# Kernel optimization log

Measured on AMD Instinct MI355X. Metric: run time of the kernel, lower is better.

## Reference

```python
import jax, jax.numpy as jnp
import numpy as np

F = 16      # frames
NV = 4096   # visual points per frame
NT = 512    # tactile points per frame
M = 4096    # model points
SCALE = 0.1


def setup_inputs() -> dict:
    key = jax.random.key(0)
    ks = jax.random.split(key, 6)
    return {
        "state": jax.random.normal(ks[0], (6,), dtype=jnp.float32) * 0.1,
        "model_points": jax.random.normal(ks[1], (M, 3), dtype=jnp.float32),
        "visual_points": jax.random.normal(ks[2], (F, NV, 3), dtype=jnp.float32),
        "tactile_points": jax.random.normal(ks[3], (F, NT, 3), dtype=jnp.float32),
        "physics_pred_states": jax.random.normal(ks[4], (F, 12), dtype=jnp.float32) * 0.1,
        "delta_time": jax.random.uniform(ks[5], (F,), dtype=jnp.float32, minval=0.01, maxval=0.05),
    }


def _skew(a):
    z = jnp.zeros((), a.dtype)
    return jnp.array([[z, -a[2], a[1]],
                      [a[2], z, -a[0]],
                      [-a[1], a[0], z]])


def _rot_from_omega(omega, dt):
    # Rodrigues: R = I + sin(theta*dt) S + (1 - cos(theta*dt)) S@S, S = skew(omega/|omega|)
    theta = jnp.linalg.norm(omega)
    ax = omega / jnp.clip(theta, 1e-8)
    S = _skew(ax)
    return jnp.eye(3, dtype=omega.dtype) + jnp.sin(theta * dt) * S + (1.0 - jnp.cos(theta * dt)) * (S @ S)


def _chamfer(pred, gt):
    # rows: pred [N,3], cols: gt [M,3]; row-min of squared distances, then mean
    d = (jnp.sum(pred * pred, axis=1)[:, None]
         + jnp.sum(gt * gt, axis=1)[None, :]
         - 2.0 * pred @ gt.T)
    return jnp.mean(jnp.min(d, axis=1))


def reference(state, model_points, visual_points, tactile_points, physics_pred_states, delta_time):
    t0 = state[:3]
    r0 = _rot_from_omega(state[3:], jnp.float32(1.0))  # Euler2Mat modeled as axis-angle

    def pose_step(carry, x):
        t, r = carry
        v, omega, dt = x
        t = t + v * dt
        r = _rot_from_omega(omega, dt) @ r
        return (t, r), (t, r)

    _, (ts, rs) = jax.lax.scan(
        pose_step, (t0, r0),
        (physics_pred_states[1:, 6:9], physics_pred_states[1:, 9:12], delta_time[1:]))
    ts = jnp.concatenate([t0[None], ts], axis=0)  # [F,3]
    rs = jnp.concatenate([r0[None], rs], axis=0)  # [F,3,3]

    def frame_loss(acc, x):
        t, r, vp, tp = x
        vc = ((vp - t) @ r) / SCALE
        tc = ((tp - t) @ r) / SCALE
        acc = acc + _chamfer(vc, model_points) + 0.1 * _chamfer(tc, model_points)
        return acc, None

    E_cd, _ = jax.lax.scan(frame_loss, jnp.zeros((), jnp.float32),
                           (ts, rs, visual_points, tactile_points))
    return E_cd
```

## Files before the change

### kernel.cpp

```cpp
#include <hip/hip_runtime.h>
#include <math.h>

#define F_    16
#define NV_   4096
#define NT_   512
#define M_    4096
#define PPF_  (NV_ + NT_)
#define NPTS_ (F_ * PPF_)
#define SCALE_INV 10.0f

#define TPB    256
#define PPT    4
#define PPB    (TPB * PPT)
#define NPB    (NPTS_ / PPB)
#define CHUNK  256
#define NCHUNK (M_ / CHUNK)

__device__ inline void rot_from_omega(float ox, float oy, float oz, float dt,
                                      float* R) {
    float theta = sqrtf(ox * ox + oy * oy + oz * oz);
    float inv = 1.0f / fmaxf(theta, 1e-8f);
    float ax = ox * inv, ay = oy * inv, az = oz * inv;
    float s = sinf(theta * dt);
    float c = 1.0f - cosf(theta * dt);
    R[0] = 1.0f - c * (ay * ay + az * az);
    R[1] = -s * az + c * ax * ay;
    R[2] =  s * ay + c * ax * az;
    R[3] =  s * az + c * ax * ay;
    R[4] = 1.0f - c * (ax * ax + az * az);
    R[5] = -s * ax + c * ay * az;
    R[6] = -s * ay + c * ax * az;
    R[7] =  s * ax + c * ay * az;
    R[8] = 1.0f - c * (ax * ax + ay * ay);
}

__device__ inline void compute_pose(int f, const float* state, const float* phys,
                                    const float* dts, float* t, float* R) {
    t[0] = state[0]; t[1] = state[1]; t[2] = state[2];
    rot_from_omega(state[3], state[4], state[5], 1.0f, R);
    for (int i = 1; i <= f; ++i) {
        float dt = dts[i];
        t[0] += phys[i * 12 + 6] * dt;
        t[1] += phys[i * 12 + 7] * dt;
        t[2] += phys[i * 12 + 8] * dt;
        float Rs[9];
        rot_from_omega(phys[i * 12 + 9], phys[i * 12 + 10], phys[i * 12 + 11], dt, Rs);
        float Rn[9];
        for (int r = 0; r < 3; ++r)
            for (int c2 = 0; c2 < 3; ++c2)
                Rn[r * 3 + c2] = Rs[r * 3 + 0] * R[0 + c2] +
                                 Rs[r * 3 + 1] * R[3 + c2] +
                                 Rs[r * 3 + 2] * R[6 + c2];
        for (int j = 0; j < 9; ++j) R[j] = Rn[j];
    }
}

__global__ void pose_kernel(const float* __restrict__ state,
                            const float* __restrict__ phys,
                            const float* __restrict__ dts,
                            float* __restrict__ poses) {
    int f = threadIdx.x;
    if (f < F_) {
        float t[3], R[9];
        compute_pose(f, state, phys, dts, t, R);
        float* o = poses + f * 12;
        o[0] = t[0]; o[1] = t[1]; o[2] = t[2];
        for (int j = 0; j < 9; ++j) o[3 + j] = R[j];
    }
}

__global__ __launch_bounds__(TPB) void chamfer_main(
    const float* __restrict__ model, const float* __restrict__ vis,
    const float* __restrict__ tac, const float* __restrict__ poses,
    float* __restrict__ partials) {
    __shared__ float4 sfeat[CHUNK];
    const int pb = blockIdx.x;
    const int ch = blockIdx.y;
    const int mbase = ch * CHUNK;

    for (int i = threadIdx.x; i < CHUNK; i += TPB) {
        float gx = model[(mbase + i) * 3 + 0];
        float gy = model[(mbase + i) * 3 + 1];
        float gz = model[(mbase + i) * 3 + 2];
        sfeat[i] = make_float4(-2.0f * gx, -2.0f * gy, -2.0f * gz,
                               gx * gx + gy * gy + gz * gz);
    }

    float c0[PPT], c1[PPT], c2[PPT], cn[PPT], dm[PPT];
    int pts[PPT];
#pragma unroll
    for (int k = 0; k < PPT; ++k) {
        int pt = pb * PPB + k * TPB + threadIdx.x;
        pts[k] = pt;
        int f = pt / PPF_;
        int loc = pt - f * PPF_;
        const float* p = (loc < NV_) ? (vis + ((size_t)f * NV_ + loc) * 3)
                                     : (tac + ((size_t)f * NT_ + (loc - NV_)) * 3);
        float px = p[0], py = p[1], pz = p[2];
        const float* ps = poses + f * 12;
        float d0 = px - ps[0], d1 = py - ps[1], d2 = pz - ps[2];
        const float* R = ps + 3;
        float x = (d0 * R[0] + d1 * R[3] + d2 * R[6]) * SCALE_INV;
        float y = (d0 * R[1] + d1 * R[4] + d2 * R[7]) * SCALE_INV;
        float z = (d0 * R[2] + d1 * R[5] + d2 * R[8]) * SCALE_INV;
        c0[k] = x; c1[k] = y; c2[k] = z;
        cn[k] = x * x + y * y + z * z;
        dm[k] = 3.4e38f;
    }
    __syncthreads();

#pragma unroll 2
    for (int m = 0; m < CHUNK; m += 2) {
        float4 ga = sfeat[m];
        float4 gb = sfeat[m + 1];
#pragma unroll
        for (int k = 0; k < PPT; ++k) {
            float da = fmaf(ga.x, c0[k], fmaf(ga.y, c1[k], fmaf(ga.z, c2[k], ga.w)));
            float db = fmaf(gb.x, c0[k], fmaf(gb.y, c1[k], fmaf(gb.z, c2[k], gb.w)));
            dm[k] = fminf(dm[k], fminf(da, db));
        }
    }

#pragma unroll
    for (int k = 0; k < PPT; ++k)
        partials[(size_t)ch * NPTS_ + pts[k]] = dm[k] + cn[k];
}

__global__ __launch_bounds__(TPB) void chamfer_reduce(
    const float* __restrict__ partials, float* __restrict__ out) {
    int pt = blockIdx.x * TPB + threadIdx.x;
    float m = partials[pt];
    for (int ch = 1; ch < NCHUNK; ++ch)
        m = fminf(m, partials[(size_t)ch * NPTS_ + pt]);
    int loc = pt % PPF_;
    float w = (loc < NV_) ? (1.0f / NV_) : (0.1f / NT_);
    float v = m * w;
#pragma unroll
    for (int off = 32; off > 0; off >>= 1) v += __shfl_down(v, off);
    __shared__ float sw[TPB / 64];
    if ((threadIdx.x & 63) == 0) sw[threadIdx.x >> 6] = v;
    __syncthreads();
    if (threadIdx.x == 0) {
        float s = 0.0f;
        for (int i = 0; i < TPB / 64; ++i) s += sw[i];
        atomicAdd(out, s);
    }
}

__global__ __launch_bounds__(TPB) void chamfer_fused(
    const float* __restrict__ state, const float* __restrict__ model,
    const float* __restrict__ vis, const float* __restrict__ tac,
    const float* __restrict__ phys, const float* __restrict__ dts,
    float* __restrict__ out) {
    __shared__ float4 sfeat[CHUNK];
    __shared__ float sposes[F_ * 12];
    __shared__ float sw[TPB / 64];

    if (threadIdx.x < F_) {
        float t[3], R[9];
        compute_pose(threadIdx.x, state, phys, dts, t, R);
        float* o = sposes + threadIdx.x * 12;
        o[0] = t[0]; o[1] = t[1]; o[2] = t[2];
        for (int j = 0; j < 9; ++j) o[3 + j] = R[j];
    }
    __syncthreads();

    float c0[PPT], c1[PPT], c2[PPT], cn[PPT], dm[PPT], wt[PPT];
#pragma unroll
    for (int k = 0; k < PPT; ++k) {
        int pt = blockIdx.x * PPB + k * TPB + threadIdx.x;
        int f = pt / PPF_;
        int loc = pt - f * PPF_;
        wt[k] = (loc < NV_) ? (1.0f / NV_) : (0.1f / NT_);
        const float* p = (loc < NV_) ? (vis + ((size_t)f * NV_ + loc) * 3)
                                     : (tac + ((size_t)f * NT_ + (loc - NV_)) * 3);
        float px = p[0], py = p[1], pz = p[2];
        const float* ps = sposes + f * 12;
        float d0 = px - ps[0], d1 = py - ps[1], d2 = pz - ps[2];
        const float* R = ps + 3;
        float x = (d0 * R[0] + d1 * R[3] + d2 * R[6]) * SCALE_INV;
        float y = (d0 * R[1] + d1 * R[4] + d2 * R[7]) * SCALE_INV;
        float z = (d0 * R[2] + d1 * R[5] + d2 * R[8]) * SCALE_INV;
        c0[k] = x; c1[k] = y; c2[k] = z;
        cn[k] = x * x + y * y + z * z;
        dm[k] = 3.4e38f;
    }

    for (int ch = 0; ch < NCHUNK; ++ch) {
        __syncthreads();
        for (int i = threadIdx.x; i < CHUNK; i += TPB) {
            int mi = ch * CHUNK + i;
            float gx = model[mi * 3 + 0], gy = model[mi * 3 + 1], gz = model[mi * 3 + 2];
            sfeat[i] = make_float4(-2.0f * gx, -2.0f * gy, -2.0f * gz,
                                   gx * gx + gy * gy + gz * gz);
        }
        __syncthreads();
#pragma unroll 2
        for (int m = 0; m < CHUNK; m += 2) {
            float4 ga = sfeat[m];
            float4 gb = sfeat[m + 1];
#pragma unroll
            for (int k = 0; k < PPT; ++k) {
                float da = fmaf(ga.x, c0[k], fmaf(ga.y, c1[k], fmaf(ga.z, c2[k], ga.w)));
                float db = fmaf(gb.x, c0[k], fmaf(gb.y, c1[k], fmaf(gb.z, c2[k], gb.w)));
                dm[k] = fminf(dm[k], fminf(da, db));
            }
        }
    }

    float v = 0.0f;
#pragma unroll
    for (int k = 0; k < PPT; ++k) v += (dm[k] + cn[k]) * wt[k];
#pragma unroll
    for (int off = 32; off > 0; off >>= 1) v += __shfl_down(v, off);
    if ((threadIdx.x & 63) == 0) sw[threadIdx.x >> 6] = v;
    __syncthreads();
    if (threadIdx.x == 0) {
        float s = 0.0f;
        for (int i = 0; i < TPB / 64; ++i) s += sw[i];
        atomicAdd(out, s);
    }
}

extern "C" void kernel_launch(void* const* d_in, const int* in_sizes, int n_in,
                              void* d_out, int out_size, void* d_ws, size_t ws_size,
                              hipStream_t stream) {
    const float* state = (const float*)d_in[0];
    const float* model = (const float*)d_in[1];
    const float* vis   = (const float*)d_in[2];
    const float* tac   = (const float*)d_in[3];
    const float* phys  = (const float*)d_in[4];
    const float* dts   = (const float*)d_in[5];
    float* out = (float*)d_out;

    hipMemsetAsync(out, 0, sizeof(float), stream);

    const size_t partial_bytes = (size_t)NCHUNK * NPTS_ * sizeof(float);
    const size_t need = partial_bytes + F_ * 12 * sizeof(float);

    if (ws_size >= need) {
        float* partials = (float*)d_ws;
        float* poses = (float*)((char*)d_ws + partial_bytes);
        pose_kernel<<<1, 64, 0, stream>>>(state, phys, dts, poses);
        dim3 grid(NPB, NCHUNK);
        chamfer_main<<<grid, TPB, 0, stream>>>(model, vis, tac, poses, partials);
        chamfer_reduce<<<NPTS_ / TPB, TPB, 0, stream>>>(partials, out);
    } else {
        chamfer_fused<<<NPB, TPB, 0, stream>>>(state, model, vis, tac, phys, dts, out);
    }
}
```

Before: 107.4 us.

## Fold pose computation into chamfer kernel and retile points per thread and chunks

Removes the separate pose kernel launch: each chamfer_main block now computes all frame poses into shared memory itself. Points per thread double to raise register reuse of each shared model point, and the model chunk halves, so the grid gains twice as many chunk blocks along y. The partials buffer grows accordingly and the reduce kernel reads twice as many chunk partials per point. Redundant per-block pose computation and higher register pressure are the costs.

```diff
diff --git a/kernel.cpp b/kernel.cpp
--- a/kernel.cpp
+++ b/kernel.cpp
@@ -10,10 +10,10 @@
 #define SCALE_INV 10.0f
 
 #define TPB    256
-#define PPT    4
+#define PPT    8
 #define PPB    (TPB * PPT)
 #define NPB    (NPTS_ / PPB)
-#define CHUNK  256
+#define CHUNK  128
 #define NCHUNK (M_ / CHUNK)
 
 __device__ inline void rot_from_omega(float ox, float oy, float oz, float dt,
@@ -55,49 +55,45 @@
     }
 }
 
-__global__ void pose_kernel(const float* __restrict__ state,
-                            const float* __restrict__ phys,
-                            const float* __restrict__ dts,
-                            float* __restrict__ poses) {
-    int f = threadIdx.x;
-    if (f < F_) {
-        float t[3], R[9];
-        compute_pose(f, state, phys, dts, t, R);
-        float* o = poses + f * 12;
-        o[0] = t[0]; o[1] = t[1]; o[2] = t[2];
-        for (int j = 0; j < 9; ++j) o[3 + j] = R[j];
-    }
-}
-
 __global__ __launch_bounds__(TPB) void chamfer_main(
-    const float* __restrict__ model, const float* __restrict__ vis,
-    const float* __restrict__ tac, const float* __restrict__ poses,
+    const float* __restrict__ state, const float* __restrict__ model,
+    const float* __restrict__ vis, const float* __restrict__ tac,
+    const float* __restrict__ phys, const float* __restrict__ dts,
     float* __restrict__ partials) {
     __shared__ float4 sfeat[CHUNK];
+    __shared__ float sposes[F_ * 12];
     const int pb = blockIdx.x;
     const int ch = blockIdx.y;
     const int mbase = ch * CHUNK;
 
-    for (int i = threadIdx.x; i < CHUNK; i += TPB) {
+    if (threadIdx.x < F_) {
+        float t[3], R[9];
+        compute_pose(threadIdx.x, state, phys, dts, t, R);
+        float* o = sposes + threadIdx.x * 12;
+        o[0] = t[0]; o[1] = t[1]; o[2] = t[2];
+        for (int j = 0; j < 9; ++j) o[3 + j] = R[j];
+    }
+
+    if (threadIdx.x < CHUNK) {
+        int i = threadIdx.x;
         float gx = model[(mbase + i) * 3 + 0];
         float gy = model[(mbase + i) * 3 + 1];
         float gz = model[(mbase + i) * 3 + 2];
         sfeat[i] = make_float4(-2.0f * gx, -2.0f * gy, -2.0f * gz,
                                gx * gx + gy * gy + gz * gz);
     }
+    __syncthreads();
 
     float c0[PPT], c1[PPT], c2[PPT], cn[PPT], dm[PPT];
-    int pts[PPT];
 #pragma unroll
     for (int k = 0; k < PPT; ++k) {
         int pt = pb * PPB + k * TPB + threadIdx.x;
-        pts[k] = pt;
         int f = pt / PPF_;
         int loc = pt - f * PPF_;
         const float* p = (loc < NV_) ? (vis + ((size_t)f * NV_ + loc) * 3)
                                      : (tac + ((size_t)f * NT_ + (loc - NV_)) * 3);
         float px = p[0], py = p[1], pz = p[2];
-        const float* ps = poses + f * 12;
+        const float* ps = sposes + f * 12;
         float d0 = px - ps[0], d1 = py - ps[1], d2 = pz - ps[2];
         const float* R = ps + 3;
         float x = (d0 * R[0] + d1 * R[3] + d2 * R[6]) * SCALE_INV;
@@ -107,9 +103,8 @@
         cn[k] = x * x + y * y + z * z;
         dm[k] = 3.4e38f;
     }
-    __syncthreads();
-
-#pragma unroll 2
+
+#pragma unroll 4
     for (int m = 0; m < CHUNK; m += 2) {
         float4 ga = sfeat[m];
         float4 gb = sfeat[m + 1];
@@ -122,8 +117,10 @@
     }
 
 #pragma unroll
-    for (int k = 0; k < PPT; ++k)
-        partials[(size_t)ch * NPTS_ + pts[k]] = dm[k] + cn[k];
+    for (int k = 0; k < PPT; ++k) {
+        int pt = pb * PPB + k * TPB + threadIdx.x;
+        partials[(size_t)ch * NPTS_ + pt] = dm[k] + cn[k];
+    }
 }
 
 __global__ __launch_bounds__(TPB) void chamfer_reduce(
@@ -147,6 +144,10 @@
     }
 }
 
+#define FB_PPT  2
+#define FB_PPB  (TPB * FB_PPT)
+#define FB_NPB  (NPTS_ / FB_PPB)
+
 __global__ __launch_bounds__(TPB) void chamfer_fused(
     const float* __restrict__ state, const float* __restrict__ model,
     const float* __restrict__ vis, const float* __restrict__ tac,
@@ -165,10 +166,10 @@
     }
     __syncthreads();
 
-    float c0[PPT], c1[PPT], c2[PPT], cn[PPT], dm[PPT], wt[PPT];
-#pragma unroll
-    for (int k = 0; k < PPT; ++k) {
-        int pt = blockIdx.x * PPB + k * TPB + threadIdx.x;
+    float c0[FB_PPT], c1[FB_PPT], c2[FB_PPT], cn[FB_PPT], dm[FB_PPT], wt[FB_PPT];
+#pragma unroll
+    for (int k = 0; k < FB_PPT; ++k) {
+        int pt = blockIdx.x * FB_PPB + k * TPB + threadIdx.x;
         int f = pt / PPF_;
         int loc = pt - f * PPF_;
         wt[k] = (loc < NV_) ? (1.0f / NV_) : (0.1f / NT_);
@@ -188,19 +189,20 @@
 
     for (int ch = 0; ch < NCHUNK; ++ch) {
         __syncthreads();
-        for (int i = threadIdx.x; i < CHUNK; i += TPB) {
+        if (threadIdx.x < CHUNK) {
+            int i = threadIdx.x;
             int mi = ch * CHUNK + i;
             float gx = model[mi * 3 + 0], gy = model[mi * 3 + 1], gz = model[mi * 3 + 2];
             sfeat[i] = make_float4(-2.0f * gx, -2.0f * gy, -2.0f * gz,
                                    gx * gx + gy * gy + gz * gz);
         }
         __syncthreads();
-#pragma unroll 2
+#pragma unroll 4
         for (int m = 0; m < CHUNK; m += 2) {
             float4 ga = sfeat[m];
             float4 gb = sfeat[m + 1];
 #pragma unroll
-            for (int k = 0; k < PPT; ++k) {
+            for (int k = 0; k < FB_PPT; ++k) {
                 float da = fmaf(ga.x, c0[k], fmaf(ga.y, c1[k], fmaf(ga.z, c2[k], ga.w)));
                 float db = fmaf(gb.x, c0[k], fmaf(gb.y, c1[k], fmaf(gb.z, c2[k], gb.w)));
                 dm[k] = fminf(dm[k], fminf(da, db));
@@ -210,7 +212,7 @@
 
     float v = 0.0f;
 #pragma unroll
-    for (int k = 0; k < PPT; ++k) v += (dm[k] + cn[k]) * wt[k];
+    for (int k = 0; k < FB_PPT; ++k) v += (dm[k] + cn[k]) * wt[k];
 #pragma unroll
     for (int off = 32; off > 0; off >>= 1) v += __shfl_down(v, off);
     if ((threadIdx.x & 63) == 0) sw[threadIdx.x >> 6] = v;
@@ -236,16 +238,15 @@
     hipMemsetAsync(out, 0, sizeof(float), stream);
 
     const size_t partial_bytes = (size_t)NCHUNK * NPTS_ * sizeof(float);
-    const size_t need = partial_bytes + F_ * 12 * sizeof(float);
-
-    if (ws_size >= need) {
+
+    if (ws_size >= partial_bytes) {
         float* partials = (float*)d_ws;
-        float* poses = (float*)((char*)d_ws + partial_bytes);
-        pose_kernel<<<1, 64, 0, stream>>>(state, phys, dts, poses);
         dim3 grid(NPB, NCHUNK);
-        chamfer_main<<<grid, TPB, 0, stream>>>(model, vis, tac, poses, partials);
+        chamfer_main<<<grid, TPB, 0, stream>>>(state, model, vis, tac, phys, dts,
+                                               partials);
         chamfer_reduce<<<NPTS_ / TPB, TPB, 0, stream>>>(partials, out);
     } else {
-        chamfer_fused<<<NPB, TPB, 0, stream>>>(state, model, vis, tac, phys, dts, out);
-    }
-}
+        chamfer_fused<<<FB_NPB, TPB, 0, stream>>>(state, model, vis, tac, phys, dts,
+                                                  out);
+    }
+}
```

Result: slower. 115.9 us (+7.9%).
